# Kernel tuning notes

Measured on AMD Instinct MI355X. Metric: run time of the kernel, lower is better.

The kernel has to match this reference:

```python
import jax, jax.numpy as jnp
import numpy as np

B, T, P, E, H, VP2, L, V = 64, 32, 64, 512, 512, 16, 16, 30000
IN = E + VP2 + L + H + E  # 1568 = LSTMCell input width


def setup_inputs() -> dict:
    key = jax.random.key(0)
    ks = list(jax.random.split(key, 24))
    it = iter(ks)
    n = lambda shape, s: jax.random.normal(next(it), shape, jnp.float32) * s
    return {
        "image": n((B, P, E), 1.0),
        "view_position": n((B, VP2), 1.0),
        "label": jax.random.uniform(next(it), (B, L), jnp.float32),
        "topic": n((B, E), 1.0),
        "temp": jnp.ones((B, 1), jnp.float32),
        "text": jax.random.randint(next(it), (B, T), 0, V),
        "word_emb": n((V, E), 0.05),
        "fc_v_w": n((H, E), 0.05), "fc_v_b": jnp.zeros((H,), jnp.float32),
        "fc_h_w": n((H, E), 0.05), "fc_h_b": jnp.zeros((H,), jnp.float32),
        "fc_m_w": n((H, E), 0.05), "fc_m_b": jnp.zeros((H,), jnp.float32),
        "w_ih": n((4 * H, IN), 0.02), "w_hh": n((4 * H, H), 0.02),
        "b_ih": jnp.zeros((4 * H,), jnp.float32), "b_hh": jnp.zeros((4 * H,), jnp.float32),
        "fc_w": n((2 * E, H), 0.05), "fc_b": jnp.zeros((2 * E,), jnp.float32),
        "fc_hh_w": n((H, E), 0.05), "fc_hh_b": jnp.zeros((H,), jnp.float32),
        "fc_s_w": n((H, E), 0.05), "fc_s_b": jnp.zeros((H,), jnp.float32),
        "fc_z_w": n((1, H), 0.05), "fc_z_b": jnp.zeros((1,), jnp.float32),
        "fc_p_w": n((V, E), 0.05), "fc_p_b": jnp.zeros((V,), jnp.float32),
    }


def reference(image, view_position, label, topic, temp, word_emb,
              fc_v_w, fc_v_b, fc_h_w, fc_h_b, fc_m_w, fc_m_b,
              w_ih, w_hh, b_ih, b_hh, fc_w, fc_b,
              fc_hh_w, fc_hh_b, fc_s_w, fc_s_b, fc_z_w, fc_z_b,
              fc_p_w, fc_p_b, text):
    # Init (dropout=0 / eval mode)
    image_mean = image.mean(1)                                   # [B,E]
    v = jnp.einsum('bpe,he->bph', image, fc_v_w) + fc_v_b        # [B,P,H]
    h0 = jnp.tanh(image_mean @ fc_h_w.T + fc_h_b)                # [B,H]
    m0 = jnp.tanh(image_mean @ fc_m_w.T + fc_m_b)                # [B,H]

    # teacher forcing ratio = 1.0: input token at step t is text[:, t-1], BOS (=0) at t=0
    bos = jnp.zeros((B, 1), text.dtype)
    toks = jnp.concatenate([bos, text[:, :-1]], axis=1).T        # [T,B]

    def step(carry, tok):
        h, m = carry
        emb = word_emb[tok]                                      # [B,E]
        x = jnp.concatenate([image_mean, view_position, label, topic, emb], axis=1)
        gates = x @ w_ih.T + b_ih + h @ w_hh.T + b_hh            # [B,4H]
        i, f, g, o = jnp.split(gates, 4, axis=1)                 # torch LSTMCell gate order
        m_new = jax.nn.sigmoid(f) * m + jax.nn.sigmoid(i) * jnp.tanh(g)
        h_new = jax.nn.sigmoid(o) * jnp.tanh(m_new)
        hs = jax.nn.relu(h_new @ fc_w.T + fc_b)                  # [B,2E]
        hh, s = hs[:, :E], hs[:, E:]
        _hh = hh @ fc_hh_w.T + fc_hh_b                           # [B,H]
        _s = s @ fc_s_w.T + fc_s_b                               # [B,H]
        ext = jnp.concatenate([v, _s[:, None, :]], axis=1)       # [B,P+1,H]
        z = jnp.tanh(ext + _hh[:, None, :])
        z = jnp.einsum('bph,h->bp', z, fc_z_w[0]) + fc_z_b[0]    # [B,P+1]
        a = jax.nn.softmax(z, axis=1)                            # attention weights
        feats = jnp.concatenate([image, s[:, None, :]], axis=1)  # [B,P+1,E]
        c = jnp.einsum('bp,bpe->be', a, feats)                   # context [B,E]
        logit = ((c + hh) @ fc_p_w.T + fc_p_b) / temp            # [B,V]
        logp = jax.nn.log_softmax(logit, axis=1)
        return (h_new, m_new), (a, logp)

    _, (attn, logp) = jax.lax.scan(step, (h0, m0), toks)
    logp_bt = logp.transpose(1, 0, 2)                            # [B,T,V]
    attn_bt = attn.transpose(1, 0, 2)                            # [B,T,P+1]
    # __sample_text=False -> _text = argmax; log_prob(argmax) = max log prob
    sum_log_prob = jnp.max(logp, axis=2).sum(0)                  # [B]
    return logp_bt, attn_bt, sum_log_prob
```

## Files before the change

kernel.cpp:

```cpp
#include <hip/hip_runtime.h>


typedef unsigned short bf16u;
typedef __attribute__((ext_vector_type(8))) short short8;
typedef __attribute__((ext_vector_type(4))) float floatx4;

#define DEV __device__ __forceinline__

DEV float b2f(bf16u u) { return __uint_as_float(((unsigned)u) << 16); }
DEV bf16u f2b(float f) {
  unsigned u = __float_as_uint(f);
  u = (u + 0x7fffu + ((u >> 16) & 1u)) >> 16;
  return (bf16u)u;
}

DEV float ftanh(float x) {
  float e = __expf(2.0f * x);
  float r = __builtin_amdgcn_rcpf(e + 1.0f);
  return __builtin_fmaf(-2.0f, r, 1.0f);
}
DEV float fsigm(float x) {
  return __builtin_amdgcn_rcpf(1.0f + __expf(-x));
}

__global__ __launch_bounds__(256)
void cvt_kernel(const float* __restrict__ src, bf16u* __restrict__ dst, int n)
{
  int i = blockIdx.x * 256 + threadIdx.x;
  if (i < n) dst[i] = f2b(src[i]);
}

__global__ __launch_bounds__(256)
void mean_kernel(const float* __restrict__ image, float* __restrict__ imean)
{
  int b = blockIdx.x;
  for (int e = threadIdx.x; e < 512; e += 256) {
    float s = 0.f;
    for (int p = 0; p < 64; ++p) s += image[(size_t)(b * 64 + p) * 512 + e];
    imean[b * 512 + e] = s * (1.0f / 64.0f);
  }
}

__global__ __launch_bounds__(256)
void prep_kernel(const float* __restrict__ imean, const float* __restrict__ vp,
                 const float* __restrict__ lab, const float* __restrict__ topic,
                 const int* __restrict__ text, const float* __restrict__ wemb,
                 bf16u* __restrict__ X)
{
  int b = blockIdx.x;
  for (int t = 0; t < 32; ++t) {
    bf16u* xr = X + ((size_t)t * 64 + b) * 1568;
    int tok = (t == 0) ? 0 : text[b * 32 + t - 1];
    for (int e = threadIdx.x; e < 512; e += 256) {
      xr[e] = f2b(imean[b * 512 + e]);
      xr[544 + e] = f2b(topic[b * 512 + e]);
      xr[1056 + e] = f2b(wemb[(size_t)tok * 512 + e]);
    }
    if (threadIdx.x < 16) {
      xr[512 + threadIdx.x] = f2b(vp[b * 16 + threadIdx.x]);
      xr[528 + threadIdx.x] = f2b(lab[b * 16 + threadIdx.x]);
    }
  }
}

__global__ __launch_bounds__(256)
void pack_whh(const float* __restrict__ whh, bf16u* __restrict__ wpack)
{
  int idx = blockIdx.x * 256 + threadIdx.x;
  int gr = idx >> 9, k = idx & 511;
  int gate = gr >> 9, win = gr & 511;
  int blk = win >> 4, lc = win & 15;
  int rr = gate * 16 + lc;
  wpack[(size_t)blk * 32768 + (((k >> 3) * 64 + rr) << 3) + (k & 7)] =
      f2b(whh[(size_t)gr * 512 + k]);
}

#define BK 32
#define LDT 40

template<int MODE>
__global__ __launch_bounds__(256)
void gemm_bt(const bf16u* __restrict__ A, int lda,
             const bf16u* __restrict__ W, int ldw,
             const float* __restrict__ bias1, const float* __restrict__ bias2,
             bf16u* __restrict__ C, int ldc,
             int M, int N, int K, int act,
             const float* __restrict__ temp,
             float* __restrict__ outbase,
             float* __restrict__ pmax, float* __restrict__ psum)
{
  __shared__ __align__(16) bf16u As[128 * LDT];
  __shared__ __align__(16) bf16u Ws[128 * LDT];
  const int tid = threadIdx.x;
  const int n0 = blockIdx.x * 128;
  const int m0 = blockIdx.y * 128;
  const int wave = tid >> 6, lane = tid & 63;
  const int wm = wave >> 1, wn = wave & 1;
  const int q = lane >> 4, l16 = lane & 15;
  const int r0 = tid >> 2, s0 = tid & 3;

  const floatx4 zero = {0.f, 0.f, 0.f, 0.f};
  floatx4 acc[4][4];
#pragma unroll
  for (int i = 0; i < 4; ++i)
#pragma unroll
    for (int j = 0; j < 4; ++j) acc[i][j] = zero;

  int ar0 = m0 + r0;      if (ar0 >= M) ar0 = M - 1;
  int ar1 = m0 + r0 + 64; if (ar1 >= M) ar1 = M - 1;
  int wr0 = n0 + r0;      if (wr0 >= N) wr0 = N - 1;
  int wr1 = n0 + r0 + 64; if (wr1 >= N) wr1 = N - 1;
  const bf16u* Ap0 = A + (size_t)ar0 * lda + s0 * 8;
  const bf16u* Ap1 = A + (size_t)ar1 * lda + s0 * 8;
  const bf16u* Wp0 = W + (size_t)wr0 * ldw + s0 * 8;
  const bf16u* Wp1 = W + (size_t)wr1 * ldw + s0 * 8;

  for (int k0 = 0; k0 < K; k0 += BK) {
    const int4 a0 = *(const int4*)(Ap0 + k0);
    const int4 a1 = *(const int4*)(Ap1 + k0);
    const int4 w0 = *(const int4*)(Wp0 + k0);
    const int4 w1 = *(const int4*)(Wp1 + k0);
    __syncthreads();
    *(int4*)(As + r0 * LDT + s0 * 8) = a0;
    *(int4*)(As + (r0 + 64) * LDT + s0 * 8) = a1;
    *(int4*)(Ws + r0 * LDT + s0 * 8) = w0;
    *(int4*)(Ws + (r0 + 64) * LDT + s0 * 8) = w1;
    __syncthreads();
    short8 af[4], wf[4];
#pragma unroll
    for (int i = 0; i < 4; ++i) {
      af[i] = *(const short8*)(As + (wm * 64 + i * 16 + l16) * LDT + q * 8);
      wf[i] = *(const short8*)(Ws + (wn * 64 + i * 16 + l16) * LDT + q * 8);
    }
#pragma unroll
    for (int i = 0; i < 4; ++i)
#pragma unroll
      for (int j = 0; j < 4; ++j)
        acc[i][j] = __builtin_amdgcn_mfma_f32_16x16x32_bf16(af[i], wf[j], acc[i][j], 0, 0, 0);
  }

  int colb[4]; float bias[4];
#pragma unroll
  for (int j = 0; j < 4; ++j) {
    int col = n0 + wn * 64 + j * 16 + l16;
    colb[j] = col;
    int cc = col < N ? col : N - 1;
    float bv = 0.f;
    if (bias1) bv += bias1[cc];
    if (bias2) bv += bias2[cc];
    bias[j] = bv;
  }

  if (MODE == 2) {
#pragma unroll
    for (int i = 0; i < 4; ++i) {
#pragma unroll
      for (int r = 0; r < 4; ++r) {
        int row = m0 + wm * 64 + i * 16 + q * 4 + r;
        if (row < M) {
#pragma unroll
          for (int j = 0; j < 4; ++j) {
            int col = colb[j];
            if (col < N) {
              float v = acc[i][j][r] + bias[j];
              if (act == 1) v = fmaxf(v, 0.f);
              C[(size_t)row * ldc + col] = f2b(v);
            }
          }
        }
      }
    }
  } else {
    int pc = blockIdx.x * 2 + wn;
#pragma unroll
    for (int i = 0; i < 4; ++i) {
#pragma unroll
      for (int r = 0; r < 4; ++r) {
        int row = m0 + wm * 64 + i * 16 + q * 4 + r;
        int bb = row & 63, tt = row >> 6;
        float rt = 1.0f / temp[bb];
        float vals[4];
#pragma unroll
        for (int j = 0; j < 4; ++j) {
          int col = colb[j];
          float v = (acc[i][j][r] + bias[j]) * rt;
          if (col < N) {
            outbase[(size_t)bb * 960000 + (size_t)tt * 30000 + col] = v;
            vals[j] = v;
          } else vals[j] = -1e30f;
        }
        float mx = fmaxf(fmaxf(vals[0], vals[1]), fmaxf(vals[2], vals[3]));
#pragma unroll
        for (int off = 1; off < 16; off <<= 1) mx = fmaxf(mx, __shfl_xor(mx, off));
        float s = 0.f;
#pragma unroll
        for (int j = 0; j < 4; ++j)
          s += (vals[j] > -1e29f) ? __expf(vals[j] - mx) : 0.f;
#pragma unroll
        for (int off = 1; off < 16; off <<= 1) s += __shfl_xor(s, off);
        if (l16 == 0) {
          pmax[(size_t)row * 470 + pc] = mx;
          psum[(size_t)row * 470 + pc] = s;
        }
      }
    }
  }
}

template<int ROWS>
__global__ void gemm_tmpl(const float* __restrict__ A, int lda,
                          const float* __restrict__ W, int ldw,
                          const float* __restrict__ bias1,
                          float* __restrict__ C, int ldc,
                          int M, int N, int K, int act)
{
  constexpr int RP = ROWS + 4;
  extern __shared__ __align__(16) float Ash[];
  const int tid = threadIdx.x;
  const int m0 = blockIdx.y * ROWS;
  const int n0 = blockIdx.x * 256;
  for (int idx = tid; idx < ROWS * K; idx += 256) {
    int r = idx / K, k = idx - r * K;
    int rr = m0 + r; if (rr >= M) rr = M - 1;
    Ash[k * RP + r] = A[(size_t)rr * lda + k];
  }
  __syncthreads();
  int n = n0 + tid;
  if (n >= N) return;
  float acc[ROWS];
#pragma unroll
  for (int r = 0; r < ROWS; ++r) acc[r] = 0.f;
  const float* wr = W + (size_t)n * ldw;
  for (int k = 0; k < K; ++k) {
    float w = wr[k];
    const float* a = Ash + (size_t)k * RP;
#pragma unroll
    for (int r = 0; r < ROWS; ++r) acc[r] += w * a[r];
  }
  float bv = bias1 ? bias1[n] : 0.f;
#pragma unroll
  for (int r = 0; r < ROWS; ++r) {
    int row = m0 + r;
    if (row < M) {
      float v = acc[r] + bv;
      if (act == 1) v = fmaxf(v, 0.f);
      else if (act == 2) v = tanhf(v);
      C[(size_t)row * ldc + n] = v;
    }
  }
}

__global__ __launch_bounds__(256)
void init_state(const float* __restrict__ h0b, const float* __restrict__ m0b,
                bf16u* __restrict__ hOut, float* __restrict__ mbuf)
{
  int i = blockIdx.x * 256 + threadIdx.x;
  int b = i >> 9, jj = i & 511;
  hOut[(((jj >> 3) * 64 + b) << 3) + (jj & 7)] = f2b(h0b[i]);
  mbuf[i] = m0b[i];
}

__global__ __launch_bounds__(256)
void lstm_step(const bf16u* __restrict__ wpack, const bf16u* __restrict__ gx,
               const bf16u* __restrict__ hIn, bf16u* __restrict__ hOut,
               float* __restrict__ mbuf, bf16u* __restrict__ h_all, int t)
{
  extern __shared__ __align__(16) char smem[];
  bf16u* hsh = (bf16u*)smem;
  bf16u* wsh = (bf16u*)(smem + 65536);
  float* gsh = (float*)(smem + 131072);
  const int blk = blockIdx.x, tid = threadIdx.x;

  const int4* hsrc = (const int4*)hIn;
  const int4* wsrc = (const int4*)(wpack + (size_t)blk * 32768);
  int4* hdst = (int4*)hsh; int4* wdst = (int4*)wsh;
#pragma unroll
  for (int u = 0; u < 16; ++u) {
    hdst[tid + 256 * u] = hsrc[tid + 256 * u];
    wdst[tid + 256 * u] = wsrc[tid + 256 * u];
  }
  __syncthreads();

  const int wave = tid >> 6, lane = tid & 63;
  const int wm = wave >> 1, wn = wave & 1, q = lane >> 4, l16 = lane & 15;
  const floatx4 zero = {0.f, 0.f, 0.f, 0.f};
  floatx4 acc[2][2];
#pragma unroll
  for (int i = 0; i < 2; ++i)
#pragma unroll
    for (int j = 0; j < 2; ++j) acc[i][j] = zero;

  for (int s = 0; s < 16; ++s) {
    short8 af[2], wf[2];
#pragma unroll
    for (int i = 0; i < 2; ++i)
      af[i] = *(const short8*)(hsh + ((((s * 4 + q) * 64) + wm * 32 + i * 16 + l16) << 3));
#pragma unroll
    for (int j = 0; j < 2; ++j)
      wf[j] = *(const short8*)(wsh + ((((s * 4 + q) * 64) + wn * 32 + j * 16 + l16) << 3));
#pragma unroll
    for (int i = 0; i < 2; ++i)
#pragma unroll
      for (int j = 0; j < 2; ++j)
        acc[i][j] = __builtin_amdgcn_mfma_f32_16x16x32_bf16(af[i], wf[j], acc[i][j], 0, 0, 0);
  }
#pragma unroll
  for (int i = 0; i < 2; ++i)
#pragma unroll
    for (int j = 0; j < 2; ++j)
#pragma unroll
      for (int r = 0; r < 4; ++r)
        gsh[(wn * 32 + j * 16 + l16) * 65 + (wm * 32 + i * 16 + q * 4 + r)] = acc[i][j][r];
  __syncthreads();

#pragma unroll
  for (int u = 0; u < 4; ++u) {
    int p = tid + 256 * u;
    int b = p >> 4, lc = p & 15;
    int jj = blk * 16 + lc;
    const bf16u* gxr = gx + ((size_t)t * 64 + b) * 2048;
    float ai = gsh[(lc) * 65 + b]        + b2f(gxr[jj]);
    float af = gsh[(16 + lc) * 65 + b]   + b2f(gxr[512 + jj]);
    float ag = gsh[(32 + lc) * 65 + b]   + b2f(gxr[1024 + jj]);
    float ao = gsh[(48 + lc) * 65 + b]   + b2f(gxr[1536 + jj]);
    float iv = fsigm(ai);
    float fv = fsigm(af);
    float gv = ftanh(ag);
    float ov = fsigm(ao);
    float mm = fv * mbuf[b * 512 + jj] + iv * gv;
    float hn = ov * ftanh(mm);
    mbuf[b * 512 + jj] = mm;
    bf16u hb = f2b(hn);
    hOut[(((jj >> 3) * 64 + b) << 3) + (jj & 7)] = hb;
    h_all[((size_t)t * 64 + b) * 512 + jj] = hb;
  }
}

__global__ __launch_bounds__(256)
void attn_kernel(const bf16u* __restrict__ vbuf, const float* __restrict__ image,
                 const bf16u* __restrict__ hs_bf, const bf16u* __restrict__ hh2,
                 const bf16u* __restrict__ s2, const float* __restrict__ wz,
                 const float* __restrict__ zb, float* __restrict__ attn_out,
                 bf16u* __restrict__ ctx)
{
  const int rown = blockIdx.x;
  const int bb = rown & 63, tt = rown >> 6;
  const int tid = threadIdx.x;
  const int wave = tid >> 6, lane = tid & 63;

  __shared__ float2 hwz[512];
  __shared__ float zpart[64][4];
  __shared__ float spart[4];
  __shared__ float ash[66];
  __shared__ float4 cpart[128];

  float sv0, sv1;
  {
    unsigned hr = *(const unsigned*)(hh2 + (size_t)rown * 512 + tid * 2);
    unsigned sr = *(const unsigned*)(s2 + (size_t)rown * 512 + tid * 2);
    float2 w2 = *(const float2*)(wz + tid * 2);
    hwz[tid * 2]     = make_float2(b2f((bf16u)(hr & 0xffffu)), w2.x);
    hwz[tid * 2 + 1] = make_float2(b2f((bf16u)(hr >> 16)), w2.y);
    sv0 = b2f((bf16u)(sr & 0xffffu));
    sv1 = b2f((bf16u)(sr >> 16));
  }
  __syncthreads();

  {
    const bf16u* vrow = vbuf + (size_t)(bb * 64 + lane) * 512 + wave * 128;
    float acc = 0.f;
    for (int c = 0; c < 16; ++c) {
      short8 vv = *(const short8*)(vrow + c * 8);
#pragma unroll
      for (int e = 0; e < 8; ++e) {
        float2 hz = hwz[wave * 128 + c * 8 + e];
        float tn = ftanh(b2f((bf16u)vv[e]) + hz.x);
        acc = __builtin_fmaf(tn, hz.y, acc);
      }
    }
    zpart[lane][wave] = acc;
  }

  {
    float2 h0 = hwz[tid * 2], h1 = hwz[tid * 2 + 1];
    float sacc = ftanh(sv0 + h0.x) * h0.y + ftanh(sv1 + h1.x) * h1.y;
#pragma unroll
    for (int off = 1; off < 64; off <<= 1) sacc += __shfl_xor(sacc, off);
    if (lane == 0) spart[wave] = sacc;
  }
  __syncthreads();

  if (wave == 0) {
    float zbv = zb[0];
    float4 zp = *(const float4*)zpart[lane];
    float z = zp.x + zp.y + zp.z + zp.w + zbv;
    float zs = spart[0] + spart[1] + spart[2] + spart[3] + zbv;
    float m = fmaxf(z, zs);
#pragma unroll
    for (int off = 1; off < 64; off <<= 1) m = fmaxf(m, __shfl_xor(m, off));
    float ez = __expf(z - m);
    float es = __expf(zs - m);
    float ssum = ez + (lane == 0 ? es : 0.f);
#pragma unroll
    for (int off = 1; off < 64; off <<= 1) ssum += __shfl_xor(ssum, off);
    float inv = 1.0f / ssum;
    ash[lane] = ez * inv;
    if (lane == 0) ash[64] = es * inv;
  }
  __syncthreads();

  size_t aoff = (size_t)bb * 2080 + (size_t)tt * 65;
  if (tid < 65) attn_out[aoff + tid] = ash[tid];

  const int e4 = tid & 127;
  const int ph = tid >> 7;
  float4 cacc = {0.f, 0.f, 0.f, 0.f};
  const float* img = image + ((size_t)bb * 64 + (size_t)ph * 32) * 512 + e4 * 4;
  for (int p = 0; p < 32; ++p) {
    float a = ash[ph * 32 + p];
    float4 iv = *(const float4*)(img + (size_t)p * 512);
    cacc.x = __builtin_fmaf(a, iv.x, cacc.x);
    cacc.y = __builtin_fmaf(a, iv.y, cacc.y);
    cacc.z = __builtin_fmaf(a, iv.z, cacc.z);
    cacc.w = __builtin_fmaf(a, iv.w, cacc.w);
  }
  if (ph == 1) cpart[e4] = cacc;
  __syncthreads();
  if (ph == 0) {
    float4 o = cpart[e4];
    cacc.x += o.x; cacc.y += o.y; cacc.z += o.z; cacc.w += o.w;
    const bf16u* hsrow = hs_bf + (size_t)rown * 1024;
    int2 hraw = *(const int2*)(hsrow + e4 * 4);
    int2 sraw = *(const int2*)(hsrow + 512 + e4 * 4);
    float a64 = ash[64];
    cacc.x += a64 * b2f((bf16u)(sraw.x & 0xffff)) + b2f((bf16u)(hraw.x & 0xffff));
    cacc.y += a64 * b2f((bf16u)((unsigned)sraw.x >> 16)) + b2f((bf16u)((unsigned)hraw.x >> 16));
    cacc.z += a64 * b2f((bf16u)(sraw.y & 0xffff)) + b2f((bf16u)(hraw.y & 0xffff));
    cacc.w += a64 * b2f((bf16u)((unsigned)sraw.y >> 16)) + b2f((bf16u)((unsigned)hraw.y >> 16));
    unsigned o0 = (unsigned)f2b(cacc.x) | ((unsigned)f2b(cacc.y) << 16);
    unsigned o1 = (unsigned)f2b(cacc.z) | ((unsigned)f2b(cacc.w) << 16);
    *(int2*)(ctx + (size_t)rown * 512 + e4 * 4) = make_int2((int)o0, (int)o1);
  }
}

__global__ __launch_bounds__(256)
void reduce_lse(const float* __restrict__ pmax, const float* __restrict__ psum,
                float* __restrict__ lse, float* __restrict__ rmax)
{
  int row = blockIdx.x * 4 + (threadIdx.x >> 6);
  int lane = threadIdx.x & 63;
  const float* pm = pmax + (size_t)row * 470;
  const float* ps = psum + (size_t)row * 470;
  float m = -1e30f, s = 0.f;
  for (int c = lane; c < 470; c += 64) {
    float mi = pm[c];
    float si = ps[c];
    if (mi > m) { s = s * __expf(m - mi) + si; m = mi; }
    else        { s += si * __expf(mi - m); }
  }
#pragma unroll
  for (int off = 1; off < 64; off <<= 1) {
    float mo = __shfl_xor(m, off);
    float so = __shfl_xor(s, off);
    float mn = fmaxf(m, mo);
    s = s * __expf(m - mn) + so * __expf(mo - mn);
    m = mn;
  }
  if (lane == 0) {
    rmax[row] = m;
    lse[row] = m + logf(s);
  }
}

__global__ __launch_bounds__(256)
void finalize_kernel(float* __restrict__ out, const float* __restrict__ lse)
{
  int idx = blockIdx.x * 256 + threadIdx.x;
  if (idx >= 15360000) return;
  int rflat = idx / 7500;
  int c4 = idx - rflat * 7500;
  float L = lse[(rflat & 31) * 64 + (rflat >> 5)];
  float4* p = (float4*)(out + (size_t)rflat * 30000 + (size_t)c4 * 4);
  float4 v = *p;
  v.x -= L; v.y -= L; v.z -= L; v.w -= L;
  *p = v;
}

__global__ void slp_kernel(const float* __restrict__ rmax,
                           const float* __restrict__ lse, float* __restrict__ out)
{
  int b = threadIdx.x;
  float s = 0.f;
  for (int t = 0; t < 32; ++t) { int r = t * 64 + b; s += rmax[r] - lse[r]; }
  out[61440000 + 133120 + b] = s;
}

extern "C" void kernel_launch(void* const* d_in, const int* in_sizes, int n_in,
                              void* d_out, int out_size, void* d_ws, size_t ws_size,
                              hipStream_t stream)
{
  const float* image   = (const float*)d_in[0];
  const float* vp      = (const float*)d_in[1];
  const float* lab     = (const float*)d_in[2];
  const float* topic   = (const float*)d_in[3];
  const float* temp    = (const float*)d_in[4];
  const int*   text    = (const int*)d_in[5];
  const float* wemb    = (const float*)d_in[6];
  const float* fc_v_w  = (const float*)d_in[7];
  const float* fc_v_b  = (const float*)d_in[8];
  const float* fc_h_w  = (const float*)d_in[9];
  const float* fc_h_b  = (const float*)d_in[10];
  const float* fc_m_w  = (const float*)d_in[11];
  const float* fc_m_b  = (const float*)d_in[12];
  const float* w_ih    = (const float*)d_in[13];
  const float* w_hh    = (const float*)d_in[14];
  const float* b_ih    = (const float*)d_in[15];
  const float* b_hh    = (const float*)d_in[16];
  const float* fc_w    = (const float*)d_in[17];
  const float* fc_b    = (const float*)d_in[18];
  const float* fc_hh_w = (const float*)d_in[19];
  const float* fc_hh_b = (const float*)d_in[20];
  const float* fc_s_w  = (const float*)d_in[21];
  const float* fc_s_b  = (const float*)d_in[22];
  const float* fc_z_w  = (const float*)d_in[23];
  const float* fc_z_b  = (const float*)d_in[24];
  const float* fc_p_w  = (const float*)d_in[25];
  const float* fc_p_b  = (const float*)d_in[26];
  float* out = (float*)d_out;

  char* base = (char*)d_ws;
  size_t off = 0;
  auto alloc = [&](size_t bytes) -> char* {
    char* p = base + off;
    off += (bytes + 255) & ~(size_t)255;
    return p;
  };
  bf16u* X       = (bf16u*)alloc(2048ull * 1568 * 2);
  bf16u* w_ih_bf = (bf16u*)alloc(2048ull * 1568 * 2);
  bf16u* gx_bf   = (bf16u*)alloc(2048ull * 2048 * 2);
  bf16u* image_bf= (bf16u*)alloc(4096ull * 512 * 2);
  bf16u* wpackb  = (bf16u*)alloc(2048ull * 512 * 2);
  bf16u* fcv_bf  = (bf16u*)alloc(512ull * 512 * 2);
  bf16u* fcw_bf  = (bf16u*)alloc(1024ull * 512 * 2);
  bf16u* fchh_bf = (bf16u*)alloc(512ull * 512 * 2);
  bf16u* fcs_bf  = (bf16u*)alloc(512ull * 512 * 2);
  bf16u* fcp_bf  = (bf16u*)alloc(30000ull * 512 * 2);
  float* imean   = (float*)alloc(64ull * 512 * 4);
  float* h0b     = (float*)alloc(64ull * 512 * 4);
  float* m0b     = (float*)alloc(64ull * 512 * 4);
  bf16u* vbuf    = (bf16u*)alloc(4096ull * 512 * 2);
  bf16u* hA      = (bf16u*)alloc(64ull * 512 * 2);
  bf16u* hB      = (bf16u*)alloc(64ull * 512 * 2);
  float* mbuf    = (float*)alloc(64ull * 512 * 4);
  bf16u* h_all   = (bf16u*)alloc(2048ull * 512 * 2);
  float* rmaxb   = (float*)alloc(2048ull * 4);
  float* lseb    = (float*)alloc(2048ull * 4);
  bf16u* hs_bf   = (bf16u*)w_ih_bf;
  bf16u* ctx     = (bf16u*)(w_ih_bf + 2048ull * 1024);
  bf16u* hhbuf   = (bf16u*)X;
  bf16u* sbuf    = (bf16u*)(X + 2048ull * 512);
  float* pmaxb   = (float*)gx_bf;
  float* psumb   = (float*)(gx_bf + 2048ull * 2048);
  (void)in_sizes; (void)n_in; (void)out_size; (void)ws_size;

  mean_kernel<<<64, 256, 0, stream>>>(image, imean);
  prep_kernel<<<64, 256, 0, stream>>>(imean, vp, lab, topic, text, wemb, X);
  cvt_kernel<<<12544, 256, 0, stream>>>(w_ih, w_ih_bf, 2048 * 1568);
  cvt_kernel<<<8192, 256, 0, stream>>>(image, image_bf, 4096 * 512);
  cvt_kernel<<<1024, 256, 0, stream>>>(fc_v_w, fcv_bf, 512 * 512);
  cvt_kernel<<<2048, 256, 0, stream>>>(fc_w, fcw_bf, 1024 * 512);
  cvt_kernel<<<1024, 256, 0, stream>>>(fc_hh_w, fchh_bf, 512 * 512);
  cvt_kernel<<<1024, 256, 0, stream>>>(fc_s_w, fcs_bf, 512 * 512);
  cvt_kernel<<<60000, 256, 0, stream>>>(fc_p_w, fcp_bf, 30000 * 512);
  pack_whh<<<4096, 256, 0, stream>>>(w_hh, wpackb);

  gemm_bt<2><<<dim3(16, 16), 256, 0, stream>>>(X, 1568, w_ih_bf, 1568, b_ih, b_hh,
      gx_bf, 2048, 2048, 2048, 1568, 0, nullptr, nullptr, nullptr, nullptr);
  gemm_bt<2><<<dim3(4, 32), 256, 0, stream>>>(image_bf, 512, fcv_bf, 512, fc_v_b, nullptr,
      vbuf, 512, 4096, 512, 512, 0, nullptr, nullptr, nullptr, nullptr);
  gemm_tmpl<32><<<dim3(2, 2), 256, 512 * 36 * 4, stream>>>(
      imean, 512, fc_h_w, 512, fc_h_b, h0b, 512, 64, 512, 512, 2);
  gemm_tmpl<32><<<dim3(2, 2), 256, 512 * 36 * 4, stream>>>(
      imean, 512, fc_m_w, 512, fc_m_b, m0b, 512, 64, 512, 512, 2);

  init_state<<<128, 256, 0, stream>>>(h0b, m0b, hA, mbuf);
  const int lstm_lds = 65536 + 65536 + 64 * 65 * 4;
  for (int t = 0; t < 32; ++t) {
    const bf16u* hi = (t & 1) ? hB : hA;
    bf16u* ho = (t & 1) ? hA : hB;
    lstm_step<<<32, 256, lstm_lds, stream>>>(wpackb, gx_bf, hi, ho, mbuf, h_all, t);
  }

  gemm_bt<2><<<dim3(8, 16), 256, 0, stream>>>(h_all, 512, fcw_bf, 512, fc_b, nullptr,
      hs_bf, 1024, 2048, 1024, 512, 1, nullptr, nullptr, nullptr, nullptr);
  gemm_bt<2><<<dim3(4, 16), 256, 0, stream>>>(hs_bf, 1024, fchh_bf, 512, fc_hh_b, nullptr,
      hhbuf, 512, 2048, 512, 512, 0, nullptr, nullptr, nullptr, nullptr);
  gemm_bt<2><<<dim3(4, 16), 256, 0, stream>>>(hs_bf + 512, 1024, fcs_bf, 512, fc_s_b, nullptr,
      sbuf, 512, 2048, 512, 512, 0, nullptr, nullptr, nullptr, nullptr);

  attn_kernel<<<2048, 256, 0, stream>>>(vbuf, image, hs_bf, hhbuf, sbuf,
      fc_z_w, fc_z_b, out + 61440000, ctx);

  gemm_bt<1><<<dim3(235, 16), 256, 0, stream>>>(ctx, 512, fcp_bf, 512, fc_p_b, nullptr,
      nullptr, 0, 2048, 30000, 512, 0, temp, out, pmaxb, psumb);

  reduce_lse<<<512, 256, 0, stream>>>(pmaxb, psumb, lseb, rmaxb);
  finalize_kernel<<<60000, 256, 0, stream>>>(out, lseb);
  slp_kernel<<<1, 64, 0, stream>>>(rmaxb, lseb, out);
}
```

Baseline: 1.189 ms.

## Merge setup kernels and swap MFMA operands for vectorized logit epilogue

Combines the mean and prep kernels, folds all fp32-to-bf16 conversions and the w_hh packing into one large launch, and merges the two h0/m0 projection GEMMs into a single grid. The aim is to cut kernel launch overhead. In the logits GEMM (MODE 1) the MFMA operands are swapped so each lane holds four consecutive columns, which allows float4 stores of the huge logp output and bias loads, plus fewer shuffles in the row max/sum reduction. The risk is the transposed accumulator layout and float4 bias reads near the column edge, where N=30000 must stay a multiple of 4.

```diff
diff --git a/kernel.cpp b/kernel.cpp
--- a/kernel.cpp
+++ b/kernel.cpp
@@ -24,35 +24,26 @@
 }
 
 __global__ __launch_bounds__(256)
-void cvt_kernel(const float* __restrict__ src, bf16u* __restrict__ dst, int n)
-{
-  int i = blockIdx.x * 256 + threadIdx.x;
-  if (i < n) dst[i] = f2b(src[i]);
-}
-
-__global__ __launch_bounds__(256)
-void mean_kernel(const float* __restrict__ image, float* __restrict__ imean)
+void mean_prep(const float* __restrict__ image, const float* __restrict__ vp,
+               const float* __restrict__ lab, const float* __restrict__ topic,
+               const int* __restrict__ text, const float* __restrict__ wemb,
+               float* __restrict__ imean, bf16u* __restrict__ X)
 {
   int b = blockIdx.x;
+  __shared__ float ims[512];
   for (int e = threadIdx.x; e < 512; e += 256) {
     float s = 0.f;
     for (int p = 0; p < 64; ++p) s += image[(size_t)(b * 64 + p) * 512 + e];
-    imean[b * 512 + e] = s * (1.0f / 64.0f);
-  }
-}
-
-__global__ __launch_bounds__(256)
-void prep_kernel(const float* __restrict__ imean, const float* __restrict__ vp,
-                 const float* __restrict__ lab, const float* __restrict__ topic,
-                 const int* __restrict__ text, const float* __restrict__ wemb,
-                 bf16u* __restrict__ X)
-{
-  int b = blockIdx.x;
+    float v = s * (1.0f / 64.0f);
+    imean[b * 512 + e] = v;
+    ims[e] = v;
+  }
+  __syncthreads();
   for (int t = 0; t < 32; ++t) {
     bf16u* xr = X + ((size_t)t * 64 + b) * 1568;
     int tok = (t == 0) ? 0 : text[b * 32 + t - 1];
     for (int e = threadIdx.x; e < 512; e += 256) {
-      xr[e] = f2b(imean[b * 512 + e]);
+      xr[e] = f2b(ims[e]);
       xr[544 + e] = f2b(topic[b * 512 + e]);
       xr[1056 + e] = f2b(wemb[(size_t)tok * 512 + e]);
     }
@@ -64,15 +55,32 @@
 }
 
 __global__ __launch_bounds__(256)
-void pack_whh(const float* __restrict__ whh, bf16u* __restrict__ wpack)
-{
-  int idx = blockIdx.x * 256 + threadIdx.x;
-  int gr = idx >> 9, k = idx & 511;
-  int gate = gr >> 9, win = gr & 511;
-  int blk = win >> 4, lc = win & 15;
-  int rr = gate * 16 + lc;
-  wpack[(size_t)blk * 32768 + (((k >> 3) * 64 + rr) << 3) + (k & 7)] =
-      f2b(whh[(size_t)gr * 512 + k]);
+void mega_cvt(const float* __restrict__ w_ih, bf16u* __restrict__ w_ih_bf,
+              const float* __restrict__ image, bf16u* __restrict__ image_bf,
+              const float* __restrict__ fc_w, bf16u* __restrict__ fcw_bf,
+              const float* __restrict__ fc_v_w, bf16u* __restrict__ fcv_bf,
+              const float* __restrict__ fc_hh_w, bf16u* __restrict__ fchh_bf,
+              const float* __restrict__ fc_s_w, bf16u* __restrict__ fcs_bf,
+              const float* __restrict__ fc_p_w, bf16u* __restrict__ fcp_bf,
+              const float* __restrict__ whh, bf16u* __restrict__ wpack)
+{
+  int i = blockIdx.x * 256 + threadIdx.x;
+  if (i < 3211264) { w_ih_bf[i] = f2b(w_ih[i]); return; }
+  if (i < 5308416) { int j = i - 3211264; image_bf[j] = f2b(image[j]); return; }
+  if (i < 5832704) { int j = i - 5308416; fcw_bf[j] = f2b(fc_w[j]); return; }
+  if (i < 6094848) { int j = i - 5832704; fcv_bf[j] = f2b(fc_v_w[j]); return; }
+  if (i < 6356992) { int j = i - 6094848; fchh_bf[j] = f2b(fc_hh_w[j]); return; }
+  if (i < 6619136) { int j = i - 6356992; fcs_bf[j] = f2b(fc_s_w[j]); return; }
+  if (i < 21979136) { int j = i - 6619136; fcp_bf[j] = f2b(fc_p_w[j]); return; }
+  {
+    int idx = i - 21979136;
+    int gr = idx >> 9, k = idx & 511;
+    int gate = gr >> 9, win = gr & 511;
+    int blk = win >> 4, lc = win & 15;
+    int rr = gate * 16 + lc;
+    wpack[(size_t)blk * 32768 + (((k >> 3) * 64 + rr) << 3) + (k & 7)] =
+        f2b(whh[(size_t)gr * 512 + k]);
+  }
 }
 
 #define BK 32
@@ -132,26 +140,33 @@
       af[i] = *(const short8*)(As + (wm * 64 + i * 16 + l16) * LDT + q * 8);
       wf[i] = *(const short8*)(Ws + (wn * 64 + i * 16 + l16) * LDT + q * 8);
     }
-#pragma unroll
-    for (int i = 0; i < 4; ++i)
-#pragma unroll
-      for (int j = 0; j < 4; ++j)
-        acc[i][j] = __builtin_amdgcn_mfma_f32_16x16x32_bf16(af[i], wf[j], acc[i][j], 0, 0, 0);
-  }
-
-  int colb[4]; float bias[4];
-#pragma unroll
-  for (int j = 0; j < 4; ++j) {
-    int col = n0 + wn * 64 + j * 16 + l16;
-    colb[j] = col;
-    int cc = col < N ? col : N - 1;
-    float bv = 0.f;
-    if (bias1) bv += bias1[cc];
-    if (bias2) bv += bias2[cc];
-    bias[j] = bv;
+    if (MODE == 1) {
+#pragma unroll
+      for (int i = 0; i < 4; ++i)
+#pragma unroll
+        for (int j = 0; j < 4; ++j)
+          acc[i][j] = __builtin_amdgcn_mfma_f32_16x16x32_bf16(wf[i], af[j], acc[i][j], 0, 0, 0);
+    } else {
+#pragma unroll
+      for (int i = 0; i < 4; ++i)
+#pragma unroll
+        for (int j = 0; j < 4; ++j)
+          acc[i][j] = __builtin_amdgcn_mfma_f32_16x16x32_bf16(af[i], wf[j], acc[i][j], 0, 0, 0);
+    }
   }
 
   if (MODE == 2) {
+    int colb[4]; float bias[4];
+#pragma unroll
+    for (int j = 0; j < 4; ++j) {
+      int col = n0 + wn * 64 + j * 16 + l16;
+      colb[j] = col;
+      int cc = col < N ? col : N - 1;
+      float bv = 0.f;
+      if (bias1) bv += bias1[cc];
+      if (bias2) bv += bias2[cc];
+      bias[j] = bv;
+    }
 #pragma unroll
     for (int i = 0; i < 4; ++i) {
 #pragma unroll
@@ -173,81 +188,84 @@
   } else {
     int pc = blockIdx.x * 2 + wn;
 #pragma unroll
-    for (int i = 0; i < 4; ++i) {
-#pragma unroll
-      for (int r = 0; r < 4; ++r) {
-        int row = m0 + wm * 64 + i * 16 + q * 4 + r;
-        int bb = row & 63, tt = row >> 6;
-        float rt = 1.0f / temp[bb];
-        float vals[4];
-#pragma unroll
-        for (int j = 0; j < 4; ++j) {
-          int col = colb[j];
-          float v = (acc[i][j][r] + bias[j]) * rt;
-          if (col < N) {
-            outbase[(size_t)bb * 960000 + (size_t)tt * 30000 + col] = v;
-            vals[j] = v;
-          } else vals[j] = -1e30f;
-        }
-        float mx = fmaxf(fmaxf(vals[0], vals[1]), fmaxf(vals[2], vals[3]));
-#pragma unroll
-        for (int off = 1; off < 16; off <<= 1) mx = fmaxf(mx, __shfl_xor(mx, off));
-        float s = 0.f;
-#pragma unroll
-        for (int j = 0; j < 4; ++j)
-          s += (vals[j] > -1e29f) ? __expf(vals[j] - mx) : 0.f;
-#pragma unroll
-        for (int off = 1; off < 16; off <<= 1) s += __shfl_xor(s, off);
-        if (l16 == 0) {
-          pmax[(size_t)row * 470 + pc] = mx;
-          psum[(size_t)row * 470 + pc] = s;
-        }
+    for (int j = 0; j < 4; ++j) {
+      int row = m0 + wm * 64 + j * 16 + l16;
+      int bb = row & 63, tt = row >> 6;
+      float rt = 1.0f / temp[bb];
+      float4 ov[4];
+      float mx = -1e30f;
+#pragma unroll
+      for (int i = 0; i < 4; ++i) {
+        int col0 = n0 + wn * 64 + i * 16 + q * 4;
+        bool ok = col0 < N;
+        float4 bv = ok ? *(const float4*)(bias1 + col0)
+                       : make_float4(0.f, 0.f, 0.f, 0.f);
+        floatx4 a = acc[i][j];
+        float4 v;
+        v.x = ok ? (a[0] + bv.x) * rt : -1e30f;
+        v.y = ok ? (a[1] + bv.y) * rt : -1e30f;
+        v.z = ok ? (a[2] + bv.z) * rt : -1e30f;
+        v.w = ok ? (a[3] + bv.w) * rt : -1e30f;
+        ov[i] = v;
+        mx = fmaxf(mx, fmaxf(fmaxf(v.x, v.y), fmaxf(v.z, v.w)));
+        if (ok)
+          *(float4*)(outbase + (size_t)bb * 960000 + (size_t)tt * 30000 + col0) = v;
       }
-    }
-  }
-}
-
-template<int ROWS>
-__global__ void gemm_tmpl(const float* __restrict__ A, int lda,
-                          const float* __restrict__ W, int ldw,
-                          const float* __restrict__ bias1,
-                          float* __restrict__ C, int ldc,
-                          int M, int N, int K, int act)
-{
-  constexpr int RP = ROWS + 4;
-  extern __shared__ __align__(16) float Ash[];
+      mx = fmaxf(mx, __shfl_xor(mx, 16));
+      mx = fmaxf(mx, __shfl_xor(mx, 32));
+      float s = 0.f;
+#pragma unroll
+      for (int i = 0; i < 4; ++i) {
+        float4 v = ov[i];
+        s += (v.x > -1e29f) ? __expf(v.x - mx) : 0.f;
+        s += (v.y > -1e29f) ? __expf(v.y - mx) : 0.f;
+        s += (v.z > -1e29f) ? __expf(v.z - mx) : 0.f;
+        s += (v.w > -1e29f) ? __expf(v.w - mx) : 0.f;
+      }
+      s += __shfl_xor(s, 16);
+      s += __shfl_xor(s, 32);
+      if (q == 0) {
+        pmax[(size_t)row * 470 + pc] = mx;
+        psum[(size_t)row * 470 + pc] = s;
+      }
+    }
+  }
+}
+
+__global__ __launch_bounds__(256)
+void gemm_hm(const float* __restrict__ A,
+             const float* __restrict__ Wh, const float* __restrict__ bh,
+             float* __restrict__ Ch,
+             const float* __restrict__ Wm, const float* __restrict__ bm,
+             float* __restrict__ Cm)
+{
+  __shared__ float Ash[512 * 36];
+  const float* W = blockIdx.z ? Wm : Wh;
+  const float* bias = blockIdx.z ? bm : bh;
+  float* C = blockIdx.z ? Cm : Ch;
   const int tid = threadIdx.x;
-  const int m0 = blockIdx.y * ROWS;
+  const int m0 = blockIdx.y * 32;
   const int n0 = blockIdx.x * 256;
-  for (int idx = tid; idx < ROWS * K; idx += 256) {
-    int r = idx / K, k = idx - r * K;
-    int rr = m0 + r; if (rr >= M) rr = M - 1;
-    Ash[k * RP + r] = A[(size_t)rr * lda + k];
+  for (int idx = tid; idx < 32 * 512; idx += 256) {
+    int r = idx >> 9, k = idx & 511;
+    Ash[k * 36 + r] = A[(size_t)(m0 + r) * 512 + k];
   }
   __syncthreads();
   int n = n0 + tid;
-  if (n >= N) return;
-  float acc[ROWS];
-#pragma unroll
-  for (int r = 0; r < ROWS; ++r) acc[r] = 0.f;
-  const float* wr = W + (size_t)n * ldw;
-  for (int k = 0; k < K; ++k) {
+  float acc[32];
+#pragma unroll
+  for (int r = 0; r < 32; ++r) acc[r] = 0.f;
+  const float* wr = W + (size_t)n * 512;
+  for (int k = 0; k < 512; ++k) {
     float w = wr[k];
-    const float* a = Ash + (size_t)k * RP;
-#pragma unroll
-    for (int r = 0; r < ROWS; ++r) acc[r] += w * a[r];
-  }
-  float bv = bias1 ? bias1[n] : 0.f;
-#pragma unroll
-  for (int r = 0; r < ROWS; ++r) {
-    int row = m0 + r;
-    if (row < M) {
-      float v = acc[r] + bv;
-      if (act == 1) v = fmaxf(v, 0.f);
-      else if (act == 2) v = tanhf(v);
-      C[(size_t)row * ldc + n] = v;
-    }
-  }
+    const float* a = Ash + (size_t)k * 36;
+#pragma unroll
+    for (int r = 0; r < 32; ++r) acc[r] += w * a[r];
+  }
+  float bv = bias[n];
+#pragma unroll
+  for (int r = 0; r < 32; ++r)
+    C[(size_t)(m0 + r) * 512 + n] = tanhf(acc[r] + bv);
 }
 
 __global__ __launch_bounds__(256)
@@ -563,25 +581,18 @@
   float* psumb   = (float*)(gx_bf + 2048ull * 2048);
   (void)in_sizes; (void)n_in; (void)out_size; (void)ws_size;
 
-  mean_kernel<<<64, 256, 0, stream>>>(image, imean);
-  prep_kernel<<<64, 256, 0, stream>>>(imean, vp, lab, topic, text, wemb, X);
-  cvt_kernel<<<12544, 256, 0, stream>>>(w_ih, w_ih_bf, 2048 * 1568);
-  cvt_kernel<<<8192, 256, 0, stream>>>(image, image_bf, 4096 * 512);
-  cvt_kernel<<<1024, 256, 0, stream>>>(fc_v_w, fcv_bf, 512 * 512);
-  cvt_kernel<<<2048, 256, 0, stream>>>(fc_w, fcw_bf, 1024 * 512);
-  cvt_kernel<<<1024, 256, 0, stream>>>(fc_hh_w, fchh_bf, 512 * 512);
-  cvt_kernel<<<1024, 256, 0, stream>>>(fc_s_w, fcs_bf, 512 * 512);
-  cvt_kernel<<<60000, 256, 0, stream>>>(fc_p_w, fcp_bf, 30000 * 512);
-  pack_whh<<<4096, 256, 0, stream>>>(w_hh, wpackb);
+  mean_prep<<<64, 256, 0, stream>>>(image, vp, lab, topic, text, wemb, imean, X);
+  mega_cvt<<<89952, 256, 0, stream>>>(w_ih, w_ih_bf, image, image_bf,
+                                      fc_w, fcw_bf, fc_v_w, fcv_bf,
+                                      fc_hh_w, fchh_bf, fc_s_w, fcs_bf,
+                                      fc_p_w, fcp_bf, w_hh, wpackb);
 
   gemm_bt<2><<<dim3(16, 16), 256, 0, stream>>>(X, 1568, w_ih_bf, 1568, b_ih, b_hh,
       gx_bf, 2048, 2048, 2048, 1568, 0, nullptr, nullptr, nullptr, nullptr);
   gemm_bt<2><<<dim3(4, 32), 256, 0, stream>>>(image_bf, 512, fcv_bf, 512, fc_v_b, nullptr,
       vbuf, 512, 4096, 512, 512, 0, nullptr, nullptr, nullptr, nullptr);
-  gemm_tmpl<32><<<dim3(2, 2), 256, 512 * 36 * 4, stream>>>(
-      imean, 512, fc_h_w, 512, fc_h_b, h0b, 512, 64, 512, 512, 2);
-  gemm_tmpl<32><<<dim3(2, 2), 256, 512 * 36 * 4, stream>>>(
-      imean, 512, fc_m_w, 512, fc_m_b, m0b, 512, 64, 512, 512, 2);
+  gemm_hm<<<dim3(2, 2, 2), 256, 0, stream>>>(imean, fc_h_w, fc_h_b, h0b,
+                                             fc_m_w, fc_m_b, m0b);
 
   init_state<<<128, 256, 0, stream>>>(h0b, m0b, hA, mbuf);
   const int lstm_lds = 65536 + 65536 + 64 * 65 * 4;
```

Result: faster. 1.029 ms (-13.5%).
